# Kernel tuning notes

Measured on AMD Instinct MI355X. Metric: run time of the kernel, lower is better.

Reference implementation:

```python
import jax, jax.numpy as jnp
import numpy as np

B, N, DIN, D, HID, C, K = 16, 1024, 768, 512, 128, 20, 64
H = W = 32
EPS = 1e-5  # BatchNorm eps (inference mode with running stats)


def _conv(x, w, pad=0, dil=1):
    return jax.lax.conv_general_dilated(
        x, w, (1, 1), [(pad, pad), (pad, pad)],
        rhs_dilation=(dil, dil),
        dimension_numbers=('NCHW', 'OIHW', 'NCHW'))


def _bn(x, g, b, m, v):
    inv = jax.lax.rsqrt(v + EPS)
    return (x - m[None, :, None, None]) * (g * inv)[None, :, None, None] + b[None, :, None, None]


def _l2norm(x):
    n = jnp.sqrt(jnp.sum(x * x, axis=-1, keepdims=True))
    return x / jnp.maximum(n, 1e-12)  # matches F.normalize(eps=1e-12)


def setup_inputs():
    key = jax.random.key(0)
    ks = jax.random.split(key, 12)

    def conv_w(k, o, i, kh, kw):
        return jax.random.normal(k, (o, i, kh, kw), jnp.float32) / np.sqrt(i * kh * kw)

    def bn_p(k, c):
        k1, k2 = jax.random.split(k)
        return (jnp.ones(c, jnp.float32), jnp.zeros(c, jnp.float32),
                0.1 * jax.random.normal(k1, (c,), jnp.float32),
                jax.random.uniform(k2, (c,), jnp.float32, 0.5, 1.5))

    g0, b0, m0, v0 = bn_p(ks[3], D)
    gr, br, mr, vr = bn_p(ks[4], HID)
    gl, bl, ml, vl = bn_p(ks[5], HID)
    gg, bg, mg, vg = bn_p(ks[6], HID)
    gp, bp, mp, vp = bn_p(ks[7], D)
    return {
        'patch_feats': jax.random.normal(ks[0], (B, N, DIN), jnp.float32),
        'protos': _l2norm(jax.random.normal(ks[1], (C, K, D), jnp.float32)),  # hybrid protos, L2-normed as in __init__
        'w0': conv_w(ks[2], D, DIN, 1, 1), 'g0': g0, 'b0': b0, 'm0': m0, 'v0': v0,
        'wr': conv_w(ks[8], HID, D, 1, 1), 'gr': gr, 'br': br, 'mr': mr, 'vr': vr,
        'wl': conv_w(ks[9], HID, HID, 3, 3), 'gl': gl, 'bl': bl, 'ml': ml, 'vl': vl,
        'wg': conv_w(ks[10], HID, HID, 3, 3), 'gg': gg, 'bg': bg, 'mg': mg, 'vg': vg,
        'wp': conv_w(ks[11], D, 2 * HID, 1, 1), 'gp': gp, 'bp': bp, 'mp': mp, 'vp': vp,
        'wf': conv_w(jax.random.fold_in(key, 99), D, D, 1, 1),
        'bf': jnp.zeros(D, jnp.float32),
        'logit_scale': jnp.float32(10.0),
    }


def reference(patch_feats, protos, w0, g0, b0, m0, v0, wr, gr, br, mr, vr,
              wl, gl, bl, ml, vl, wg, gg, bg, mg, vg, wp, gp, bp, mp, vp,
              wf, bf, logit_scale):
    Bq, Nq, Din = patch_feats.shape
    x = patch_feats.transpose(0, 2, 1).reshape(Bq, Din, H, W)
    # adapter: 1x1 conv -> BN -> ReLU
    x = jax.nn.relu(_bn(_conv(x, w0), g0, b0, m0, v0))
    # ResidualContextBlock
    res = x
    o = jax.nn.relu(_bn(_conv(x, wr), gr, br, mr, vr))
    l = jax.nn.relu(_bn(_conv(o, wl, pad=1), gl, bl, ml, vl))
    g = jax.nn.relu(_bn(_conv(o, wg, pad=2, dil=2), gg, bg, mg, vg))
    o = _bn(_conv(jnp.concatenate([l, g], axis=1), wp), gp, bp, mp, vp)
    x = jax.nn.relu(o + res)
    # final 1x1 conv (with bias)
    x = _conv(x, wf) + bf[None, :, None, None]
    # back to [B, N, D], L2 normalize
    x = x.reshape(Bq, D, Nq).transpose(0, 2, 1)
    x = _l2norm(x)
    # per-class cosine sims + double max reduction (vectorized over classes)
    sims = jnp.einsum('bnd,ckd->bcnk', x, protos)  # [B,C,N,K]
    A = sims.max(axis=-1)                          # [B,C,N] patch->proto max
    act_maps = A.reshape(Bq, C, H, W)
    logits = A.max(axis=-1) * logit_scale          # [B,C]
    return logits, act_maps, x
```

## Files before the change

### kernel.cpp

```cpp
#include <hip/hip_runtime.h>
#include <math.h>

#define BN_EPS 1e-5f

typedef __attribute__((ext_vector_type(8))) short short8v;
typedef __attribute__((ext_vector_type(8))) unsigned short ushort8v;
typedef __attribute__((ext_vector_type(4))) float f32x4;

__device__ __forceinline__ unsigned short f2b(float f) {
    unsigned int u = __float_as_uint(f);
    return (unsigned short)((u + 0x7FFFu + ((u >> 16) & 1u)) >> 16);
}
__device__ __forceinline__ float b2f(unsigned short h) {
    return __uint_as_float(((unsigned int)h) << 16);
}

typedef __attribute__((address_space(1))) const unsigned int gas_uint;
typedef __attribute__((address_space(3))) unsigned int las_uint;
__device__ __forceinline__ void gload16(const void* g, void* l) {
    __builtin_amdgcn_global_load_lds((gas_uint*)g, (las_uint*)l, 16, 0, 0);
}

#define VMCNT4()  asm volatile("s_waitcnt vmcnt(4)"  ::: "memory")
#define VMCNT6()  asm volatile("s_waitcnt vmcnt(6)"  ::: "memory")
#define VMCNT0()  asm volatile("s_waitcnt vmcnt(0)"  ::: "memory")
#define LGKM0()   asm volatile("s_waitcnt lgkmcnt(0)" ::: "memory")
#define SBAR()    __builtin_amdgcn_s_barrier()
#define SCHED0()  __builtin_amdgcn_sched_barrier(0)

__global__ __launch_bounds__(256) void prep_all(
    const float* __restrict__ pf,  const float* __restrict__ w0,
    const float* __restrict__ wr,  const float* __restrict__ wp,
    const float* __restrict__ wf,  const float* __restrict__ prot,
    const float* __restrict__ wl,  const float* __restrict__ wg,
    unsigned short* __restrict__ pf_o, unsigned short* __restrict__ w0_o,
    unsigned short* __restrict__ wr_o, unsigned short* __restrict__ wp_o,
    unsigned short* __restrict__ wf_o, unsigned short* __restrict__ prot_o,
    unsigned short* __restrict__ wt_o, unsigned short* __restrict__ opad)
{
    int i = blockIdx.x * 256 + threadIdx.x;
    if (i >= 2129920) return;
    if (i >= 1798144) {
        ushort8v z;
#pragma unroll
        for (int k = 0; k < 8; ++k) z[k] = 0;
        *(ushort8v*)(opad + (size_t)(i - 1798144) * 8) = z;
        return;
    }
    if (i >= 1761280) {
        int e0 = (i - 1761280) * 8;
        ushort8v u;
#pragma unroll
        for (int q = 0; q < 8; ++q) {
            int e = e0 + q;
            int br = e >= 147456;
            int j  = e - br * 147456;
            int tap = j >> 14, oc = (j >> 7) & 127, ic = j & 127;
            const float* src = br ? wg : wl;
            u[q] = f2b(src[((oc << 7) + ic) * 9 + tap]);
        }
        *(ushort8v*)(wt_o + (size_t)e0) = u;
        return;
    }
    const float* src; unsigned short* dst; int off;
    if      (i <  1572864) { src = pf;   dst = pf_o;   off = i; }
    else if (i <  1622016) { src = w0;   dst = w0_o;   off = i - 1572864; }
    else if (i <  1630208) { src = wr;   dst = wr_o;   off = i - 1622016; }
    else if (i <  1646592) { src = wp;   dst = wp_o;   off = i - 1630208; }
    else if (i <  1679360) { src = wf;   dst = wf_o;   off = i - 1646592; }
    else                   { src = prot; dst = prot_o; off = i - 1679360; }
    const float4* p = (const float4*)(src + (size_t)off * 8);
    float4 a = p[0], b = p[1];
    ushort8v r;
    r[0] = f2b(a.x); r[1] = f2b(a.y); r[2] = f2b(a.z); r[3] = f2b(a.w);
    r[4] = f2b(b.x); r[5] = f2b(b.y); r[6] = f2b(b.z); r[7] = f2b(b.w);
    *(ushort8v*)(dst + (size_t)off * 8) = r;
}

template <int EPI>
__global__ __launch_bounds__(256, 3) void mfma_gemm(
    const unsigned short* __restrict__ A, int lda,
    const unsigned short* __restrict__ Wt, int ldw,
    void* __restrict__ outp, int ldc, int Kdim,
    const float* __restrict__ bng, const float* __restrict__ bnb,
    const float* __restrict__ bnm, const float* __restrict__ bnv,
    const unsigned short* __restrict__ res, int ldres,
    const float* __restrict__ bias)
{
    __shared__ short8v Asta[2][512];
    __shared__ short8v Bsta[2][512];
    const int t  = threadIdx.x;
    const int l  = t & 63, wv = t >> 6;
    const int wm = wv >> 1, wn = wv & 1;
    const int m0 = blockIdx.x << 7, n0 = blockIdx.y << 7;

    const int r0  = t & 127;
    const int kb0 = t >> 7;

    const unsigned short* Ap = A  + (size_t)(m0 + r0) * lda + kb0 * 8;
    const unsigned short* Bp = Wt + (size_t)(n0 + r0) * ldw + kb0 * 8;

    f32x4 acc[4][4];
#pragma unroll
    for (int mf = 0; mf < 4; ++mf)
#pragma unroll
        for (int nf = 0; nf < 4; ++nf)
#pragma unroll
            for (int j = 0; j < 4; ++j) acc[mf][nf][j] = 0.f;

    const int arow = wm * 64 + (l & 15);
    const int brow = wn * 64 + (l & 15);
    const int kq   = l >> 4;
    const int nK   = Kdim >> 5;

#define STAGE_G(buf, k0)                                     \
    do {                                                     \
        gload16(Ap + (k0),      &Asta[buf][wv * 64]);        \
        gload16(Ap + (k0) + 16, &Asta[buf][wv * 64 + 256]);  \
        gload16(Bp + (k0),      &Bsta[buf][wv * 64]);        \
        gload16(Bp + (k0) + 16, &Bsta[buf][wv * 64 + 256]);  \
    } while (0)

    STAGE_G(0, 0);
    int cur = 0;
    for (int ks = 0; ks < nK; ++ks) {
        if (ks + 1 < nK) { STAGE_G(cur ^ 1, (ks + 1) << 5); VMCNT4(); }
        else             { VMCNT0(); }
        SBAR();
        short8v af[4], bfv[4];
#pragma unroll
        for (int mf = 0; mf < 4; ++mf) af[mf]  = Asta[cur][kq * 128 + arow + mf * 16];
#pragma unroll
        for (int nf = 0; nf < 4; ++nf) bfv[nf] = Bsta[cur][kq * 128 + brow + nf * 16];
#pragma unroll
        for (int mf = 0; mf < 4; ++mf)
#pragma unroll
            for (int nf = 0; nf < 4; ++nf)
                acc[mf][nf] = __builtin_amdgcn_mfma_f32_16x16x32_bf16(
                    af[mf], bfv[nf], acc[mf][nf], 0, 0, 0);
        LGKM0(); SCHED0();
        SBAR();
        cur ^= 1;
    }
#undef STAGE_G

    float s[4], sh[4];
    int cols[4];
#pragma unroll
    for (int nf = 0; nf < 4; ++nf) {
        int col = n0 + wn * 64 + nf * 16 + (l & 15);
        cols[nf] = col;
        if (EPI == 2) { s[nf] = 1.f; sh[nf] = bias[col]; }
        else {
            float sc = bng[col] * rsqrtf(bnv[col] + BN_EPS);
            s[nf]  = sc;
            sh[nf] = bnb[col] - bnm[col] * sc;
        }
    }
#pragma unroll
    for (int mf = 0; mf < 4; ++mf) {
#pragma unroll
        for (int j = 0; j < 4; ++j) {
            int row = m0 + wm * 64 + mf * 16 + kq * 4 + j;
#pragma unroll
            for (int nf = 0; nf < 4; ++nf) {
                float v = acc[mf][nf][j] * s[nf] + sh[nf];
                if (EPI == 1) v += b2f(res[(size_t)row * ldres + cols[nf]]);
                if (EPI != 2) v = fmaxf(v, 0.f);
                if (EPI == 2) {
                    ((float*)outp)[(size_t)row * ldc + cols[nf]] = v;
                } else if (EPI == 3) {
                    int b = row >> 10, h = (row >> 5) & 31, ww = row & 31;
                    size_t pidx = ((size_t)(b * 36 + h + 2) * 36 + (ww + 2)) * 128 + cols[nf];
                    ((unsigned short*)outp)[pidx] = f2b(v);
                } else {
                    ((unsigned short*)outp)[(size_t)row * ldc + cols[nf]] = f2b(v);
                }
            }
        }
    }
}

__global__ __launch_bounds__(256, 3) void conv_mfma(
    const unsigned short* __restrict__ opad,
    const unsigned short* __restrict__ wt_all,
    const float* __restrict__ g1, const float* __restrict__ b1,
    const float* __restrict__ m1, const float* __restrict__ v1,
    const float* __restrict__ g2, const float* __restrict__ b2,
    const float* __restrict__ m2, const float* __restrict__ v2,
    unsigned short* __restrict__ lg)
{
    __shared__ short8v Asta[2][512];
    __shared__ short8v Bsta[2][1024];
    const int t = threadIdx.x;
    const int l = t & 63, wv = t >> 6;
    const int wm = wv >> 1, wn = wv & 1;
    const int m0 = blockIdx.x << 6;
    const int br = blockIdx.y;
    const int dil = 1 + br;
    const unsigned short* wtb = wt_all + (size_t)br * 147456;

    const int r0 = t & 63;
    const int m  = m0 + r0;
    const int bb = m >> 10, h = (m >> 5) & 31, wc = m & 31;
    const ptrdiff_t pbase = ((ptrdiff_t)(bb * 36 + h + 2) * 36 + (wc + 2)) * 128;
    const unsigned short* ApT = opad + pbase + (t >> 6) * 8;
    const unsigned short* BpT = wtb + (size_t)(t & 127) * 128 + (t >> 7) * 8;

    f32x4 acc[2][4];
#pragma unroll
    for (int mf = 0; mf < 2; ++mf)
#pragma unroll
        for (int nf = 0; nf < 4; ++nf)
#pragma unroll
            for (int j = 0; j < 4; ++j) acc[mf][nf][j] = 0.f;

    const int arow = wm * 32 + (l & 15);
    const int bcol = wn * 64 + (l & 15);
    const int kq   = l >> 4;

#define STAGE_C(buf, s)                                                        \
    do {                                                                       \
        int tap_ = (s) >> 1, hh_ = ((s) & 1) * 64;                             \
        int dh_ = tap_ / 3 - 1, dw_ = tap_ % 3 - 1;                            \
        const unsigned short* Ap_ = ApT + (ptrdiff_t)((dh_ * 36 + dw_) * dil) * 128 + hh_; \
        const unsigned short* Bp_ = BpT + (size_t)tap_ * 16384 + hh_;          \
        gload16(Ap_,      &Asta[buf][wv * 64]);                                \
        gload16(Ap_ + 32, &Asta[buf][wv * 64 + 256]);                          \
        gload16(Bp_,      &Bsta[buf][wv * 64]);                                \
        gload16(Bp_ + 16, &Bsta[buf][wv * 64 + 256]);                          \
        gload16(Bp_ + 32, &Bsta[buf][wv * 64 + 512]);                          \
        gload16(Bp_ + 48, &Bsta[buf][wv * 64 + 768]);                          \
    } while (0)

    STAGE_C(0, 0);
    int cur = 0;
    for (int s = 0; s < 18; ++s) {
        if (s + 1 < 18) { STAGE_C(cur ^ 1, s + 1); VMCNT6(); }
        else            { VMCNT0(); }
        SBAR();
        short8v af[2][2], bfv[2][4];
#pragma unroll
        for (int kk = 0; kk < 2; ++kk) {
            int kb = kk * 4 + kq;
            af[kk][0] = Asta[cur][kb * 64 + arow];
            af[kk][1] = Asta[cur][kb * 64 + arow + 16];
#pragma unroll
            for (int nf = 0; nf < 4; ++nf)
                bfv[kk][nf] = Bsta[cur][kb * 128 + bcol + nf * 16];
        }
#pragma unroll
        for (int kk = 0; kk < 2; ++kk)
#pragma unroll
            for (int mf = 0; mf < 2; ++mf)
#pragma unroll
                for (int nf = 0; nf < 4; ++nf)
                    acc[mf][nf] = __builtin_amdgcn_mfma_f32_16x16x32_bf16(
                        af[kk][mf], bfv[kk][nf], acc[mf][nf], 0, 0, 0);
        LGKM0(); SCHED0();
        SBAR();
        cur ^= 1;
    }
#undef STAGE_C

    const float* gg = br ? g2 : g1;
    const float* gb = br ? b2 : b1;
    const float* gm = br ? m2 : m1;
    const float* gv = br ? v2 : v1;
    float s4[4], sh[4];
    int cols[4];
#pragma unroll
    for (int nf = 0; nf < 4; ++nf) {
        int col = bcol + nf * 16;
        cols[nf] = col;
        float sc = gg[col] * rsqrtf(gv[col] + BN_EPS);
        s4[nf] = sc;
        sh[nf] = gb[col] - gm[col] * sc;
    }
#pragma unroll
    for (int mf = 0; mf < 2; ++mf) {
#pragma unroll
        for (int j = 0; j < 4; ++j) {
            int row = m0 + wm * 32 + mf * 16 + kq * 4 + j;
#pragma unroll
            for (int nf = 0; nf < 4; ++nf) {
                float v = fmaxf(acc[mf][nf][j] * s4[nf] + sh[nf], 0.f);
                lg[(size_t)row * 256 + br * 128 + cols[nf]] = f2b(v);
            }
        }
    }
}

__global__ __launch_bounds__(256) void l2norm_rows(
    float* __restrict__ x, unsigned short* __restrict__ xn)
{
    const int t    = threadIdx.x;
    const int wv   = t >> 6, lane = t & 63;
    const int row  = (blockIdx.x << 2) + wv;
    float* p = x + (size_t)row * 512 + (lane << 3);
    float4 a = *(float4*)p;
    float4 b = *(float4*)(p + 4);
    float ss = a.x * a.x + a.y * a.y + a.z * a.z + a.w * a.w +
               b.x * b.x + b.y * b.y + b.z * b.z + b.w * b.w;
#pragma unroll
    for (int off = 32; off >= 1; off >>= 1) ss += __shfl_xor(ss, off);
    float sc = 1.f / fmaxf(sqrtf(ss), 1e-12f);
    a.x *= sc; a.y *= sc; a.z *= sc; a.w *= sc;
    b.x *= sc; b.y *= sc; b.z *= sc; b.w *= sc;
    *(float4*)p       = a;
    *(float4*)(p + 4) = b;
    ushort8v r;
    r[0] = f2b(a.x); r[1] = f2b(a.y); r[2] = f2b(a.z); r[3] = f2b(a.w);
    r[4] = f2b(b.x); r[5] = f2b(b.y); r[6] = f2b(b.z); r[7] = f2b(b.w);
    *(ushort8v*)(xn + (size_t)row * 512 + (lane << 3)) = r;
}

__global__ __launch_bounds__(256, 3) void sims_mfma(
    const unsigned short* __restrict__ xn,
    const unsigned short* __restrict__ protos,
    float* __restrict__ act)
{
    __shared__ short8v Asta[2][512];
    __shared__ short8v Bsta[2][512];
    const int t = threadIdx.x;
    const int l = t & 63, wv = t >> 6;
    const int wm = wv >> 1, wn = wv & 1;
    const int m0 = blockIdx.x << 7;

    const int r0  = t & 127, kb0 = t >> 7;
    const unsigned short* Ap = xn + (size_t)(m0 + r0) * 512 + kb0 * 8;
    const unsigned short* Bp = protos + ((size_t)blockIdx.y * 128 + r0) * 512 + kb0 * 8;

    f32x4 acc[4][4];
#pragma unroll
    for (int mf = 0; mf < 4; ++mf)
#pragma unroll
        for (int nf = 0; nf < 4; ++nf)
#pragma unroll
            for (int j = 0; j < 4; ++j) acc[mf][nf][j] = 0.f;

    const int arow = wm * 64 + (l & 15);
    const int brow = wn * 64 + (l & 15);
    const int kq   = l >> 4;

#define STAGE_S(buf, k0)                                     \
    do {                                                     \
        gload16(Ap + (k0),      &Asta[buf][wv * 64]);        \
        gload16(Ap + (k0) + 16, &Asta[buf][wv * 64 + 256]);  \
        gload16(Bp + (k0),      &Bsta[buf][wv * 64]);        \
        gload16(Bp + (k0) + 16, &Bsta[buf][wv * 64 + 256]);  \
    } while (0)

    STAGE_S(0, 0);
    __syncthreads();
    int cur = 0;
    for (int ks = 0; ks < 16; ++ks) {
        short8v af[4], bfv[4];
#pragma unroll
        for (int mf = 0; mf < 4; ++mf) af[mf]  = Asta[cur][kq * 128 + arow + mf * 16];
#pragma unroll
        for (int nf = 0; nf < 4; ++nf) bfv[nf] = Bsta[cur][kq * 128 + brow + nf * 16];
        if (ks + 1 < 16) STAGE_S(cur ^ 1, (ks + 1) << 5);
#pragma unroll
        for (int mf = 0; mf < 4; ++mf)
#pragma unroll
            for (int nf = 0; nf < 4; ++nf)
                acc[mf][nf] = __builtin_amdgcn_mfma_f32_16x16x32_bf16(
                    af[mf], bfv[nf], acc[mf][nf], 0, 0, 0);
        __syncthreads();
        cur ^= 1;
    }
#undef STAGE_S

    const int c = (blockIdx.y << 1) + wn;
#pragma unroll
    for (int mf = 0; mf < 4; ++mf) {
        float vj[4];
#pragma unroll
        for (int j = 0; j < 4; ++j) {
            float v = fmaxf(fmaxf(acc[mf][0][j], acc[mf][1][j]),
                            fmaxf(acc[mf][2][j], acc[mf][3][j]));
            v = fmaxf(v, __shfl_xor(v, 1));
            v = fmaxf(v, __shfl_xor(v, 2));
            v = fmaxf(v, __shfl_xor(v, 4));
            v = fmaxf(v, __shfl_xor(v, 8));
            vj[j] = v;
        }
        if ((l & 15) == 0) {
            int rowb = m0 + wm * 64 + mf * 16 + kq * 4;
#pragma unroll
            for (int j = 0; j < 4; ++j) {
                int row = rowb + j;
                int bb = row >> 10, n = row & 1023;
                act[(((size_t)(bb * 20 + c)) << 10) + n] = vj[j];
            }
        }
    }
}

__global__ __launch_bounds__(256) void logits_max(
    const float* __restrict__ act, const float* __restrict__ lsc,
    float* __restrict__ logits)
{
    const int bc = blockIdx.x;
    const int t  = threadIdx.x;
    float4 v = *(const float4*)(act + ((size_t)bc << 10) + (t << 2));
    float mx = fmaxf(fmaxf(v.x, v.y), fmaxf(v.z, v.w));
#pragma unroll
    for (int off = 32; off >= 1; off >>= 1) mx = fmaxf(mx, __shfl_xor(mx, off));
    __shared__ float wmred[4];
    if ((t & 63) == 0) wmred[t >> 6] = mx;
    __syncthreads();
    if (t == 0) {
        float m2 = fmaxf(fmaxf(wmred[0], wmred[1]), fmaxf(wmred[2], wmred[3]));
        logits[bc] = m2 * lsc[0];
    }
}

extern "C" void kernel_launch(void* const* d_in, const int* in_sizes, int n_in,
                              void* d_out, int out_size, void* d_ws, size_t ws_size,
                              hipStream_t stream)
{
    const float* pf   = (const float*)d_in[0];
    const float* prot = (const float*)d_in[1];
    const float* w0   = (const float*)d_in[2];
    const float* g0   = (const float*)d_in[3];
    const float* b0   = (const float*)d_in[4];
    const float* m0v  = (const float*)d_in[5];
    const float* v0   = (const float*)d_in[6];
    const float* wr   = (const float*)d_in[7];
    const float* gr   = (const float*)d_in[8];
    const float* br   = (const float*)d_in[9];
    const float* mr   = (const float*)d_in[10];
    const float* vr   = (const float*)d_in[11];
    const float* wl   = (const float*)d_in[12];
    const float* gl   = (const float*)d_in[13];
    const float* bl   = (const float*)d_in[14];
    const float* ml   = (const float*)d_in[15];
    const float* vl   = (const float*)d_in[16];
    const float* wg   = (const float*)d_in[17];
    const float* gG   = (const float*)d_in[18];
    const float* bG   = (const float*)d_in[19];
    const float* mG   = (const float*)d_in[20];
    const float* vG   = (const float*)d_in[21];
    const float* wp   = (const float*)d_in[22];
    const float* gp   = (const float*)d_in[23];
    const float* bp   = (const float*)d_in[24];
    const float* mp   = (const float*)d_in[25];
    const float* vp   = (const float*)d_in[26];
    const float* wf   = (const float*)d_in[27];
    const float* bf_  = (const float*)d_in[28];
    const float* lsc  = (const float*)d_in[29];

    char* ws = (char*)d_ws;
    unsigned short* pf_bf    = (unsigned short*)(ws);
    unsigned short* w0_bf    = (unsigned short*)(ws + 25165824);
    unsigned short* wr_bf    = (unsigned short*)(ws + 25952256);
    unsigned short* wt_bf    = (unsigned short*)(ws + 26083328);
    unsigned short* wp_bf    = (unsigned short*)(ws + 26673152);
    unsigned short* wf_bf    = (unsigned short*)(ws + 26935296);
    unsigned short* prot_bf  = (unsigned short*)(ws + 27459584);
    unsigned short* x1_bf    = (unsigned short*)(ws + 28770304);
    unsigned short* opad     = (unsigned short*)(ws + 45547520);
    unsigned short* lg_bf    = (unsigned short*)(ws + 50855936);
    unsigned short* x2_bf    = (unsigned short*)(ws + 59244544);
    unsigned short* xn_bf    = (unsigned short*)(ws + 76021760);

    float* out    = (float*)d_out;
    float* logits = out;
    float* act    = out + 320;
    float* xo     = out + 328000;

    prep_all<<<8320, 256, 0, stream>>>(
        pf, w0, wr, wp, wf, prot, wl, wg,
        pf_bf, w0_bf, wr_bf, wp_bf, wf_bf, prot_bf, wt_bf, opad);

    mfma_gemm<0><<<dim3(128, 4), 256, 0, stream>>>(
        pf_bf, 768, w0_bf, 768, x1_bf, 512, 768,
        g0, b0, m0v, v0, nullptr, 0, nullptr);

    mfma_gemm<3><<<dim3(128, 1), 256, 0, stream>>>(
        x1_bf, 512, wr_bf, 512, opad, 0, 512,
        gr, br, mr, vr, nullptr, 0, nullptr);

    conv_mfma<<<dim3(256, 2), 256, 0, stream>>>(
        opad, wt_bf, gl, bl, ml, vl, gG, bG, mG, vG, lg_bf);

    mfma_gemm<1><<<dim3(128, 4), 256, 0, stream>>>(
        lg_bf, 256, wp_bf, 256, x2_bf, 512, 256,
        gp, bp, mp, vp, x1_bf, 512, nullptr);

    mfma_gemm<2><<<dim3(128, 4), 256, 0, stream>>>(
        x2_bf, 512, wf_bf, 512, xo, 512, 512,
        nullptr, nullptr, nullptr, nullptr, nullptr, 0, bf_);

    l2norm_rows<<<4096, 256, 0, stream>>>(xo, xn_bf);

    sims_mfma<<<dim3(128, 10), 256, 0, stream>>>(xn_bf, prot_bf, act);

    logits_max<<<320, 256, 0, stream>>>(act, lsc, logits);
}
```

Before: 195.9 us.

## Fuse fp32-to-bf16 conversion of patch features into first GEMM; retile reduce GEMM

The patch_feats fp32-to-bf16 pass in prep_all is removed. The first 1x1-conv GEMM now loads fp32 A tiles into registers, converts them to bf16 and writes them to LDS itself, which avoids writing and re-reading a 24MB bf16 copy. The HID=128 reduce GEMM moves to a new 64-row-tile kernel with 256 blocks instead of 128, to fill more compute units. The cost is that fp32 A loads go through registers and need VALU conversion inside the main loop, adding latency and register pressure.

```diff
diff --git a/kernel.cpp b/kernel.cpp
--- a/kernel.cpp
+++ b/kernel.cpp
@@ -21,6 +21,8 @@
     __builtin_amdgcn_global_load_lds((gas_uint*)g, (las_uint*)l, 16, 0, 0);
 }
 
+#define VMCNT2()  asm volatile("s_waitcnt vmcnt(2)"  ::: "memory")
+#define VMCNT3()  asm volatile("s_waitcnt vmcnt(3)"  ::: "memory")
 #define VMCNT4()  asm volatile("s_waitcnt vmcnt(4)"  ::: "memory")
 #define VMCNT6()  asm volatile("s_waitcnt vmcnt(6)"  ::: "memory")
 #define VMCNT0()  asm volatile("s_waitcnt vmcnt(0)"  ::: "memory")
@@ -29,26 +31,26 @@
 #define SCHED0()  __builtin_amdgcn_sched_barrier(0)
 
 __global__ __launch_bounds__(256) void prep_all(
-    const float* __restrict__ pf,  const float* __restrict__ w0,
-    const float* __restrict__ wr,  const float* __restrict__ wp,
-    const float* __restrict__ wf,  const float* __restrict__ prot,
+    const float* __restrict__ w0,  const float* __restrict__ wr,
+    const float* __restrict__ wp,  const float* __restrict__ wf,
+    const float* __restrict__ prot,
     const float* __restrict__ wl,  const float* __restrict__ wg,
-    unsigned short* __restrict__ pf_o, unsigned short* __restrict__ w0_o,
-    unsigned short* __restrict__ wr_o, unsigned short* __restrict__ wp_o,
-    unsigned short* __restrict__ wf_o, unsigned short* __restrict__ prot_o,
+    unsigned short* __restrict__ w0_o, unsigned short* __restrict__ wr_o,
+    unsigned short* __restrict__ wp_o, unsigned short* __restrict__ wf_o,
+    unsigned short* __restrict__ prot_o,
     unsigned short* __restrict__ wt_o, unsigned short* __restrict__ opad)
 {
     int i = blockIdx.x * 256 + threadIdx.x;
-    if (i >= 2129920) return;
-    if (i >= 1798144) {
+    if (i >= 557056) return;
+    if (i >= 225280) {
         ushort8v z;
 #pragma unroll
         for (int k = 0; k < 8; ++k) z[k] = 0;
-        *(ushort8v*)(opad + (size_t)(i - 1798144) * 8) = z;
+        *(ushort8v*)(opad + (size_t)(i - 225280) * 8) = z;
         return;
     }
-    if (i >= 1761280) {
-        int e0 = (i - 1761280) * 8;
+    if (i >= 188416) {
+        int e0 = (i - 188416) * 8;
         ushort8v u;
 #pragma unroll
         for (int q = 0; q < 8; ++q) {
@@ -63,18 +65,141 @@
         return;
     }
     const float* src; unsigned short* dst; int off;
-    if      (i <  1572864) { src = pf;   dst = pf_o;   off = i; }
-    else if (i <  1622016) { src = w0;   dst = w0_o;   off = i - 1572864; }
-    else if (i <  1630208) { src = wr;   dst = wr_o;   off = i - 1622016; }
-    else if (i <  1646592) { src = wp;   dst = wp_o;   off = i - 1630208; }
-    else if (i <  1679360) { src = wf;   dst = wf_o;   off = i - 1646592; }
-    else                   { src = prot; dst = prot_o; off = i - 1679360; }
+    if      (i <  49152) { src = w0;   dst = w0_o;   off = i; }
+    else if (i <  57344) { src = wr;   dst = wr_o;   off = i - 49152; }
+    else if (i <  73728) { src = wp;   dst = wp_o;   off = i - 57344; }
+    else if (i < 106496) { src = wf;   dst = wf_o;   off = i - 73728; }
+    else                 { src = prot; dst = prot_o; off = i - 106496; }
     const float4* p = (const float4*)(src + (size_t)off * 8);
     float4 a = p[0], b = p[1];
     ushort8v r;
     r[0] = f2b(a.x); r[1] = f2b(a.y); r[2] = f2b(a.z); r[3] = f2b(a.w);
     r[4] = f2b(b.x); r[5] = f2b(b.y); r[6] = f2b(b.z); r[7] = f2b(b.w);
     *(ushort8v*)(dst + (size_t)off * 8) = r;
+}
+
+__global__ __launch_bounds__(256, 3) void mfma_gemm_f32a(
+    const float* __restrict__ A, int lda,
+    const unsigned short* __restrict__ Wt, int ldw,
+    unsigned short* __restrict__ outp, int ldc, int Kdim,
+    const float* __restrict__ bng, const float* __restrict__ bnb,
+    const float* __restrict__ bnm, const float* __restrict__ bnv)
+{
+    __shared__ short8v Asta[2][512];
+    __shared__ short8v Bsta[2][512];
+    const int t  = threadIdx.x;
+    const int l  = t & 63, wv = t >> 6;
+    const int wm = wv >> 1, wn = wv & 1;
+    const int m0 = blockIdx.x << 7, n0 = blockIdx.y << 7;
+
+    const int r0  = t & 127;
+    const int kb0 = t >> 7;
+
+    const float*          Apf = A  + (size_t)(m0 + r0) * lda + kb0 * 8;
+    const unsigned short* Bp  = Wt + (size_t)(n0 + r0) * ldw + kb0 * 8;
+
+    f32x4 acc[4][4];
+#pragma unroll
+    for (int mf = 0; mf < 4; ++mf)
+#pragma unroll
+        for (int nf = 0; nf < 4; ++nf)
+#pragma unroll
+            for (int j = 0; j < 4; ++j) acc[mf][nf][j] = 0.f;
+
+    const int arow = wm * 64 + (l & 15);
+    const int brow = wn * 64 + (l & 15);
+    const int kq   = l >> 4;
+    const int nK   = Kdim >> 5;
+
+    float4 areg[2][2];
+
+#define LOADA(k0)                                                   \
+    do {                                                            \
+        areg[0][0] = *(const float4*)(Apf + (k0));                  \
+        areg[0][1] = *(const float4*)(Apf + (k0) + 4);              \
+        areg[1][0] = *(const float4*)(Apf + (k0) + 16);             \
+        areg[1][1] = *(const float4*)(Apf + (k0) + 20);             \
+    } while (0)
+
+#define WRITEA(buf)                                                 \
+    do {                                                            \
+        _Pragma("unroll")                                           \
+        for (int c_ = 0; c_ < 2; ++c_) {                            \
+            ushort8v u_;                                            \
+            u_[0] = f2b(areg[c_][0].x); u_[1] = f2b(areg[c_][0].y); \
+            u_[2] = f2b(areg[c_][0].z); u_[3] = f2b(areg[c_][0].w); \
+            u_[4] = f2b(areg[c_][1].x); u_[5] = f2b(areg[c_][1].y); \
+            u_[6] = f2b(areg[c_][1].z); u_[7] = f2b(areg[c_][1].w); \
+            *(ushort8v*)&Asta[buf][t + 256 * c_] = u_;              \
+        }                                                           \
+    } while (0)
+
+#define STAGEB(buf, k0)                                      \
+    do {                                                     \
+        gload16(Bp + (k0),      &Bsta[buf][wv * 64]);        \
+        gload16(Bp + (k0) + 16, &Bsta[buf][wv * 64 + 256]);  \
+    } while (0)
+
+    LOADA(0);
+    STAGEB(0, 0);
+    VMCNT2();
+    WRITEA(0);
+    VMCNT0(); LGKM0();
+    SBAR();
+
+    int cur = 0;
+    for (int ks = 0; ks < nK; ++ks) {
+        const bool more = (ks + 1 < nK);
+        if (more) {
+            LOADA((ks + 1) << 5);
+            STAGEB(cur ^ 1, (ks + 1) << 5);
+        }
+        short8v af[4], bfv[4];
+#pragma unroll
+        for (int mf = 0; mf < 4; ++mf) af[mf]  = Asta[cur][kq * 128 + arow + mf * 16];
+#pragma unroll
+        for (int nf = 0; nf < 4; ++nf) bfv[nf] = Bsta[cur][kq * 128 + brow + nf * 16];
+#pragma unroll
+        for (int mf = 0; mf < 4; ++mf)
+#pragma unroll
+            for (int nf = 0; nf < 4; ++nf)
+                acc[mf][nf] = __builtin_amdgcn_mfma_f32_16x16x32_bf16(
+                    af[mf], bfv[nf], acc[mf][nf], 0, 0, 0);
+        if (more) {
+            VMCNT2();
+            WRITEA(cur ^ 1);
+        }
+        LGKM0(); SCHED0();
+        VMCNT0();
+        SBAR();
+        cur ^= 1;
+    }
+#undef LOADA
+#undef WRITEA
+#undef STAGEB
+
+    float s[4], sh[4];
+    int cols[4];
+#pragma unroll
+    for (int nf = 0; nf < 4; ++nf) {
+        int col = n0 + wn * 64 + nf * 16 + (l & 15);
+        cols[nf] = col;
+        float sc = bng[col] * rsqrtf(bnv[col] + BN_EPS);
+        s[nf]  = sc;
+        sh[nf] = bnb[col] - bnm[col] * sc;
+    }
+#pragma unroll
+    for (int mf = 0; mf < 4; ++mf) {
+#pragma unroll
+        for (int j = 0; j < 4; ++j) {
+            int row = m0 + wm * 64 + mf * 16 + kq * 4 + j;
+#pragma unroll
+            for (int nf = 0; nf < 4; ++nf) {
+                float v = fmaxf(acc[mf][nf][j] * s[nf] + sh[nf], 0.f);
+                outp[(size_t)row * ldc + cols[nf]] = f2b(v);
+            }
+        }
+    }
 }
 
 template <int EPI>
@@ -169,13 +294,94 @@
                 if (EPI != 2) v = fmaxf(v, 0.f);
                 if (EPI == 2) {
                     ((float*)outp)[(size_t)row * ldc + cols[nf]] = v;
-                } else if (EPI == 3) {
-                    int b = row >> 10, h = (row >> 5) & 31, ww = row & 31;
-                    size_t pidx = ((size_t)(b * 36 + h + 2) * 36 + (ww + 2)) * 128 + cols[nf];
-                    ((unsigned short*)outp)[pidx] = f2b(v);
                 } else {
                     ((unsigned short*)outp)[(size_t)row * ldc + cols[nf]] = f2b(v);
                 }
+            }
+        }
+    }
+}
+
+__global__ __launch_bounds__(256, 3) void mfma_gemm64_pad(
+    const unsigned short* __restrict__ A,
+    const unsigned short* __restrict__ Wt,
+    unsigned short* __restrict__ opad,
+    const float* __restrict__ bng, const float* __restrict__ bnb,
+    const float* __restrict__ bnm, const float* __restrict__ bnv)
+{
+    __shared__ short8v Asta[2][256];
+    __shared__ short8v Bsta[2][512];
+    const int t  = threadIdx.x;
+    const int l  = t & 63, wv = t >> 6;
+    const int wm = wv >> 1, wn = wv & 1;
+    const int m0 = blockIdx.x << 6;
+
+    const unsigned short* Ap = A  + (size_t)(m0 + (t & 63)) * 512 + (t >> 6) * 8;
+    const unsigned short* Bp = Wt + (size_t)(t & 127) * 512 + (t >> 7) * 8;
+
+    f32x4 acc[2][4];
+#pragma unroll
+    for (int mf = 0; mf < 2; ++mf)
+#pragma unroll
+        for (int nf = 0; nf < 4; ++nf)
+#pragma unroll
+            for (int j = 0; j < 4; ++j) acc[mf][nf][j] = 0.f;
+
+    const int arow = wm * 32 + (l & 15);
+    const int brow = wn * 64 + (l & 15);
+    const int kq   = l >> 4;
+
+#define STAGE_R(buf, k0)                                     \
+    do {                                                     \
+        gload16(Ap + (k0),      &Asta[buf][wv * 64]);        \
+        gload16(Bp + (k0),      &Bsta[buf][wv * 64]);        \
+        gload16(Bp + (k0) + 16, &Bsta[buf][wv * 64 + 256]);  \
+    } while (0)
+
+    STAGE_R(0, 0);
+    int cur = 0;
+    for (int ks = 0; ks < 16; ++ks) {
+        if (ks + 1 < 16) { STAGE_R(cur ^ 1, (ks + 1) << 5); VMCNT3(); }
+        else             { VMCNT0(); }
+        SBAR();
+        short8v af[2], bfv[4];
+#pragma unroll
+        for (int mf = 0; mf < 2; ++mf) af[mf]  = Asta[cur][kq * 64 + arow + mf * 16];
+#pragma unroll
+        for (int nf = 0; nf < 4; ++nf) bfv[nf] = Bsta[cur][kq * 128 + brow + nf * 16];
+#pragma unroll
+        for (int mf = 0; mf < 2; ++mf)
+#pragma unroll
+            for (int nf = 0; nf < 4; ++nf)
+                acc[mf][nf] = __builtin_amdgcn_mfma_f32_16x16x32_bf16(
+                    af[mf], bfv[nf], acc[mf][nf], 0, 0, 0);
+        LGKM0(); SCHED0();
+        SBAR();
+        cur ^= 1;
+    }
+#undef STAGE_R
+
+    float s[4], sh[4];
+    int cols[4];
+#pragma unroll
+    for (int nf = 0; nf < 4; ++nf) {
+        int col = wn * 64 + nf * 16 + (l & 15);
+        cols[nf] = col;
+        float sc = bng[col] * rsqrtf(bnv[col] + BN_EPS);
+        s[nf]  = sc;
+        sh[nf] = bnb[col] - bnm[col] * sc;
+    }
+#pragma unroll
+    for (int mf = 0; mf < 2; ++mf) {
+#pragma unroll
+        for (int j = 0; j < 4; ++j) {
+            int row = m0 + wm * 32 + mf * 16 + kq * 4 + j;
+            int b = row >> 10, h = (row >> 5) & 31, ww = row & 31;
+            size_t pbase = ((size_t)(b * 36 + h + 2) * 36 + (ww + 2)) * 128;
+#pragma unroll
+            for (int nf = 0; nf < 4; ++nf) {
+                float v = fmaxf(acc[mf][nf][j] * s[nf] + sh[nf], 0.f);
+                opad[pbase + cols[nf]] = f2b(v);
             }
         }
     }
@@ -453,35 +659,32 @@
     const float* lsc  = (const float*)d_in[29];
 
     char* ws = (char*)d_ws;
-    unsigned short* pf_bf    = (unsigned short*)(ws);
-    unsigned short* w0_bf    = (unsigned short*)(ws + 25165824);
-    unsigned short* wr_bf    = (unsigned short*)(ws + 25952256);
-    unsigned short* wt_bf    = (unsigned short*)(ws + 26083328);
-    unsigned short* wp_bf    = (unsigned short*)(ws + 26673152);
-    unsigned short* wf_bf    = (unsigned short*)(ws + 26935296);
-    unsigned short* prot_bf  = (unsigned short*)(ws + 27459584);
-    unsigned short* x1_bf    = (unsigned short*)(ws + 28770304);
-    unsigned short* opad     = (unsigned short*)(ws + 45547520);
-    unsigned short* lg_bf    = (unsigned short*)(ws + 50855936);
-    unsigned short* x2_bf    = (unsigned short*)(ws + 59244544);
-    unsigned short* xn_bf    = (unsigned short*)(ws + 76021760);
+    unsigned short* w0_bf    = (unsigned short*)(ws);
+    unsigned short* wr_bf    = (unsigned short*)(ws + 786432);
+    unsigned short* wt_bf    = (unsigned short*)(ws + 917504);
+    unsigned short* wp_bf    = (unsigned short*)(ws + 1507328);
+    unsigned short* wf_bf    = (unsigned short*)(ws + 1769472);
+    unsigned short* prot_bf  = (unsigned short*)(ws + 2293760);
+    unsigned short* x1_bf    = (unsigned short*)(ws + 3604480);
+    unsigned short* opad     = (unsigned short*)(ws + 20381696);
+    unsigned short* lg_bf    = (unsigned short*)(ws + 25690112);
+    unsigned short* x2_bf    = (unsigned short*)(ws + 34078720);
+    unsigned short* xn_bf    = (unsigned short*)(ws + 50855936);
 
     float* out    = (float*)d_out;
     float* logits = out;
     float* act    = out + 320;
     float* xo     = out + 328000;
 
-    prep_all<<<8320, 256, 0, stream>>>(
-        pf, w0, wr, wp, wf, prot, wl, wg,
-        pf_bf, w0_bf, wr_bf, wp_bf, wf_bf, prot_bf, wt_bf, opad);
-
-    mfma_gemm<0><<<dim3(128, 4), 256, 0, stream>>>(
-        pf_bf, 768, w0_bf, 768, x1_bf, 512, 768,
-        g0, b0, m0v, v0, nullptr, 0, nullptr);
-
-    mfma_gemm<3><<<dim3(128, 1), 256, 0, stream>>>(
-        x1_bf, 512, wr_bf, 512, opad, 0, 512,
-        gr, br, mr, vr, nullptr, 0, nullptr);
+    prep_all<<<2176, 256, 0, stream>>>(
+        w0, wr, wp, wf, prot, wl, wg,
+        w0_bf, wr_bf, wp_bf, wf_bf, prot_bf, wt_bf, opad);
+
+    mfma_gemm_f32a<<<dim3(128, 4), 256, 0, stream>>>(
+        pf, 768, w0_bf, 768, x1_bf, 512, 768, g0, b0, m0v, v0);
+
+    mfma_gemm64_pad<<<256, 256, 0, stream>>>(
+        x1_bf, wr_bf, opad, gr, br, mr, vr);
 
     conv_mfma<<<dim3(256, 2), 256, 0, stream>>>(
         opad, wt_bf, gl, bl, ml, vl, gG, bG, mG, vG, lg_bf);
```

Result: faster. 189.4 us (-3.3%).
